# Kernel tuning notes

Measured on AMD Instinct MI355X. Metric: run time of the kernel, lower is better.

Reference implementation:

```python
import jax, jax.numpy as jnp
import numpy as np

B, D, O = 128, 1024, 512
EPS = 1e-5

def setup_inputs() -> dict:
    key = jax.random.key(0)
    ks = jax.random.split(key, 12)
    s = 0.02  # truncated-normal-ish scale
    glorot1 = float(np.sqrt(6.0 / (D + O)))
    glorot3 = float(np.sqrt(6.0 / (3 * O + O)))
    return {
        "x": jax.random.normal(ks[0], (B, D), jnp.float32),
        "gt": jax.random.normal(ks[1], (D, O), jnp.float32) * s,
        "wt": jax.random.normal(ks[2], (D, O), jnp.float32) * s,
        "mt": jax.random.normal(ks[3], (D, O), jnp.float32) * s,
        "kernel_1": jax.random.uniform(ks[4], (D, O), jnp.float32, -glorot1, glorot1),
        "bias_1": jnp.zeros((O,), jnp.float32),
        "kernel_3": jax.random.uniform(ks[5], (3 * O, O), jnp.float32, -glorot3, glorot3),
        "bias_3": jnp.zeros((O,), jnp.float32),
        "emb_kernel": jax.random.normal(ks[6], (1, 1, 3 * O), jnp.float32) * s,  # conv1d kernel [1, in=1, 3O]
        "emb_bias": jnp.zeros((3 * O,), jnp.float32),
        "embeding_k": jax.random.normal(ks[7], (1, D, 1), jnp.float32) * s,
        "norm_g": jnp.ones((O,), jnp.float32),
        "norm_b": jnp.zeros((O,), jnp.float32),
    }

def reference(x, gt, wt, mt, kernel_1, bias_1, kernel_3, bias_3,
              emb_kernel, emb_bias, embeding_k, norm_g, norm_b):
    # perceptron cell (identity activation)
    c1 = x @ kernel_1 + bias_1                                  # [B,O]
    # NALU cell
    wa = jnp.tanh(wt) * jax.nn.sigmoid(mt)                      # [D,O]
    g = jax.nn.sigmoid(x @ gt)                                  # [B,O]
    a = x @ wa                                                  # [B,O]
    m = jnp.sinh(jnp.arcsinh(x) @ wa)                           # [B,O]
    c3 = g * a + (1.0 - g) * m                                  # [B,O]
    # test cell: per-feature self-attention
    e = x[..., None] * emb_kernel.reshape(1, 1, -1) + emb_bias  # [B,D,3O]
    q, k, v = jnp.split(e, 3, axis=-1)                          # each [B,D,O]
    scale = jax.lax.rsqrt(jnp.asarray(v.shape[-1], x.dtype))
    w = jnp.einsum('bdo,beo->bde', q, k) * scale                # [B,D,D]
    w = jax.nn.softmax(w, axis=-1)
    att = jnp.einsum('bde,beo->bdo', w, v)                      # [B,D,O]
    s = jnp.sum(att * embeding_k, axis=1)                       # [B,O]
    u = jnp.mean(s, axis=-1, keepdims=True)
    var = jnp.mean(jnp.square(s - u), axis=-1, keepdims=True)
    c4 = (s - u) * jax.lax.rsqrt(var + EPS) * norm_g + norm_b   # [B,O]
    feat = jnp.concatenate([c1, c3, c4], axis=-1)               # [B,3O]
    return feat @ kernel_3 + bias_3                             # [B,O]
```

## Files before the change

### kernel.cpp

```cpp
#include <hip/hip_runtime.h>
#include <hip/hip_bf16.h>
#include <math.h>

typedef unsigned short u16;
typedef unsigned int u32;
typedef __attribute__((ext_vector_type(8))) short bf16x8;
typedef __attribute__((ext_vector_type(4))) float f32x4;

#define NB 128
#define ND 1024
#define NO 512
#define EPSV 1e-5f
#define SCALEQK 0.04419417382415922f
#define LOG2E 1.4426950408889634f

static __device__ __forceinline__ float fast_exp2(float v) {
#if __has_builtin(__builtin_amdgcn_exp2f)
  return __builtin_amdgcn_exp2f(v);
#else
  return exp2f(v);
#endif
}
static __device__ __forceinline__ float fast_rcp(float v) {
#if __has_builtin(__builtin_amdgcn_rcpf)
  return __builtin_amdgcn_rcpf(v);
#else
  return 1.f / v;
#endif
}
static __device__ __forceinline__ u16 bf16_rtn(float f) {
  unsigned u = __float_as_uint(f);
  return (u16)((u + 0x7FFFu + ((u >> 16) & 1u)) >> 16);
}
static __device__ __forceinline__ float asinh_fast(float x) {
  const float ax = fabsf(x);
  const float s = sqrtf(fmaf(ax, ax, 1.f));
  return copysignf(__logf(ax + s), x);
}
static __device__ __forceinline__ float tanh_fast(float x) {
  return 1.f - 2.f * fast_rcp(fast_exp2(x * (2.f * LOG2E)) + 1.f);
}
static __device__ __forceinline__ float sig_fast(float x) {
  return fast_rcp(1.f + fast_exp2(-x * LOG2E));
}
static __device__ __forceinline__ float sinh_fast(float x) {
  const float z = fast_exp2(x * LOG2E);
  return 0.5f * (z - fast_rcp(z));
}

template <int AMODE, int WMODE>
static __device__ __forceinline__ void gemmA_tile(
    const float* __restrict__ Xf, const float* __restrict__ W0,
    const float* __restrict__ W1, float* __restrict__ outp,
    int o0, int k0, char* smem) {
  u16* Ash = (u16*)smem;
  u16* Bsh = (u16*)(smem + 32768);
  const int t = threadIdx.x;
  const int lane = t & 63;
  const int wr = (t >> 6) & 3;
  const int wc = t >> 8;
  const f32x4 vz = {0.f, 0.f, 0.f, 0.f};
  f32x4 acc[2][2];
  acc[0][0] = vz; acc[0][1] = vz; acc[1][0] = vz; acc[1][1] = vz;

#pragma unroll
  for (int c = 0; c < 2; ++c) {
    const int kc = k0 + c * 128;
    if (c) __syncthreads();
    {
      const int rsub = t >> 5, c4 = (t & 31) * 4;
#pragma unroll
      for (int pass = 0; pass < 8; ++pass) {
        const int row = pass * 16 + rsub;
        const float4 v = *(const float4*)(Xf + (size_t)row * ND + kc + c4);
        float e[4] = {v.x, v.y, v.z, v.w};
        if (AMODE == 2) {
#pragma unroll
          for (int i = 0; i < 4; ++i) e[i] = asinh_fast(e[i]);
        }
        u16 h[4];
#pragma unroll
        for (int i = 0; i < 4; ++i) h[i] = bf16_rtn(e[i]);
        const int byte = (row * 256 + c4 * 2) ^ ((row & 7) << 4);
        *(uint2*)((char*)Ash + byte) =
            make_uint2((u32)h[0] | ((u32)h[1] << 16), (u32)h[2] | ((u32)h[3] << 16));
      }
    }
    {
      const int gkr = t >> 4, og = t & 15;
      const int go = o0 + og * 4;
#pragma unroll
      for (int kk = 0; kk < 4; ++kk) {
        const int gk = kc + gkr * 4 + kk;
        float4 w0 = *(const float4*)&W0[(size_t)gk * NO + go];
        if (WMODE) {
          const float4 m0 = *(const float4*)&W1[(size_t)gk * NO + go];
          w0.x = tanh_fast(w0.x) * sig_fast(m0.x);
          w0.y = tanh_fast(w0.y) * sig_fast(m0.y);
          w0.z = tanh_fast(w0.z) * sig_fast(m0.z);
          w0.w = tanh_fast(w0.w) * sig_fast(m0.w);
        }
        const float e[4] = {w0.x, w0.y, w0.z, w0.w};
#pragma unroll
        for (int j = 0; j < 4; ++j) {
          const int col = og * 4 + j;
          const int byte = (col * 256 + (gkr * 4 + kk) * 2) ^ ((col & 7) << 4);
          *(u16*)((char*)Bsh + byte) = bf16_rtn(e[j]);
        }
      }
    }
    __syncthreads();
#pragma unroll
    for (int ks2 = 0; ks2 < 4; ++ks2) {
      const int kbyte = ks2 * 64 + (lane >> 4) * 16;
      bf16x8 a[2], b[2];
#pragma unroll
      for (int m = 0; m < 2; ++m) {
        const int row = wr * 32 + m * 16 + (lane & 15);
        a[m] = *(const bf16x8*)((const char*)Ash + ((row * 256 + kbyte) ^ ((row & 7) << 4)));
      }
#pragma unroll
      for (int n = 0; n < 2; ++n) {
        const int col = wc * 32 + n * 16 + (lane & 15);
        b[n] = *(const bf16x8*)((const char*)Bsh + ((col * 256 + kbyte) ^ ((col & 7) << 4)));
      }
#pragma unroll
      for (int m = 0; m < 2; ++m)
#pragma unroll
        for (int n = 0; n < 2; ++n)
          acc[m][n] = __builtin_amdgcn_mfma_f32_16x16x32_bf16(a[m], b[n], acc[m][n], 0, 0, 0);
    }
  }
#pragma unroll
  for (int m = 0; m < 2; ++m)
#pragma unroll
    for (int n = 0; n < 2; ++n) {
      const int col = o0 + wc * 32 + n * 16 + (lane & 15);
#pragma unroll
      for (int r = 0; r < 4; ++r) {
        const int row = wr * 32 + m * 16 + (lane >> 4) * 4 + r;
        outp[(size_t)row * NO + col] = acc[m][n][r];
      }
    }
}

__global__ __launch_bounds__(512) void k1_fused(
    const float* __restrict__ x, const float* __restrict__ gt,
    const float* __restrict__ wt, const float* __restrict__ mt,
    const float* __restrict__ k1w, const float* __restrict__ embk,
    const float* __restrict__ embb, const float* __restrict__ ekd,
    const float* __restrict__ k3w, const float* __restrict__ ng,
    const float* __restrict__ nbv, float* __restrict__ Tfull,
    float* __restrict__ pA, float* __restrict__ U, float* __restrict__ V,
    float* __restrict__ Wc) {
  __shared__ __align__(16) char smem[49152];
  const int bid = blockIdx.x;
  const int t = threadIdx.x;
  const int wv = t >> 6;

  if (bid < NB) {
    float* xsh = (float*)smem;
    float(*red)[8] = (float(*)[8])(smem + 4096);
    float* bc = (float*)(smem + 4096 + 7 * 8 * 4);
    *(float2*)&xsh[t * 2] = *(const float2*)&x[bid * ND + t * 2];
    float s1, s3;
    {
      const float kk = embk[NO + t];
      s1 = embk[t] * kk;
      s3 = kk * embb[t];
    }
#pragma unroll
    for (int off = 32; off; off >>= 1) {
      s1 += __shfl_xor(s1, off);
      s3 += __shfl_xor(s3, off);
    }
    if ((t & 63) == 0) { red[0][wv] = s1; red[1][wv] = s3; }
    __syncthreads();
    if (t < 2) {
      float v = 0.f;
#pragma unroll
      for (int i = 0; i < 8; ++i) v += red[t][i];
      bc[t] = v;
    }
    __syncthreads();
    const float S1 = bc[0], S3 = bc[1];
    const float aL2 = SCALEQK * LOG2E * S3;
    const float dS1 = SCALEQK * S1;
    float mm[7];
#pragma unroll
    for (int k = 0; k < 7; ++k) mm[k] = 0.f;
#pragma unroll
    for (int j = 0; j < 2; ++j) {
      const float xe = xsh[t * 2 + j];
      float p = fast_exp2(aL2 * xe);
      mm[0] += p;
#pragma unroll
      for (int k = 1; k < 7; ++k) { p *= xe; mm[k] += p; }
    }
#pragma unroll
    for (int off = 32; off; off >>= 1)
#pragma unroll
      for (int k = 0; k < 7; ++k) mm[k] += __shfl_xor(mm[k], off);
    if ((t & 63) == 0)
#pragma unroll
      for (int k = 0; k < 7; ++k) red[k][wv] = mm[k];
    __syncthreads();
    if (t < 7) {
      float v = 0.f;
#pragma unroll
      for (int i = 0; i < 8; ++i) v += red[t][i];
      bc[2 + t] = v;
    }
    __syncthreads();
    const float invf[6] = {1.f, 1.f, 0.5f, 1.6666667e-1f, 4.1666668e-2f, 8.3333333e-3f};
    float cn[6], cd[6];
#pragma unroll
    for (int k = 0; k < 6; ++k) {
      cn[k] = bc[3 + k] * invf[k];
      cd[k] = bc[2 + k] * invf[k];
    }
    float Ta = 0.f;
#pragma unroll
    for (int j = 0; j < 2; ++j) {
      const int d = t * 2 + j;
      const float del = dS1 * xsh[d];
      float num = cn[5], den = cd[5];
#pragma unroll
      for (int k = 4; k >= 0; --k) {
        num = fmaf(num, del, cn[k]);
        den = fmaf(den, del, cd[k]);
      }
      Ta = fmaf(ekd[d], num / den, Ta);
    }
#pragma unroll
    for (int off = 32; off; off >>= 1) Ta += __shfl_xor(Ta, off);
    __syncthreads();
    if ((t & 63) == 0) red[0][wv] = Ta;
    __syncthreads();
    if (t == 0) {
      float v = 0.f;
#pragma unroll
      for (int i = 0; i < 8; ++i) v += red[0][i];
      Tfull[bid] = v;
    }
    return;
  }
  if (bid < 256) {
    const int b2 = bid - NB;
    const int g = b2 >> 5, ks = (b2 >> 3) & 3, ot = b2 & 7;
    float* outp = pA + (size_t)(g * 4 + ks) * (NB * NO);
    if (g == 0)
      gemmA_tile<1, 0>(x, k1w, k1w, outp, ot * 64, ks * 256, smem);
    else if (g == 1)
      gemmA_tile<1, 0>(x, gt, gt, outp, ot * 64, ks * 256, smem);
    else if (g == 2)
      gemmA_tile<1, 1>(x, wt, mt, outp, ot * 64, ks * 256, smem);
    else
      gemmA_tile<2, 1>(x, wt, mt, outp, ot * 64, ks * 256, smem);
    return;
  }
  {
    float(*lds)[64][3] = (float(*)[64][3])smem;
    __shared__ float mred[2][8];
    __shared__ float mbc[2];
    float svk = embk[2 * NO + t], svb = embb[2 * NO + t];
#pragma unroll
    for (int off = 32; off; off >>= 1) {
      svk += __shfl_xor(svk, off);
      svb += __shfl_xor(svb, off);
    }
    if ((t & 63) == 0) { mred[0][wv] = svk; mred[1][wv] = svb; }
    __syncthreads();
    if (t < 2) {
      float s = 0.f;
#pragma unroll
      for (int i = 0; i < 8; ++i) s += mred[t][i];
      mbc[t] = s * (1.f / (float)NO);
    }
    __syncthreads();
    const float mvk = mbc[0], mvb = mbc[1];
    const int jbase = (bid - 256) * 64;
    const int j = jbase + (t & 63);
    const int oc = t >> 6;
    float au = 0.f, av = 0.f, aw = 0.f;
#pragma unroll 4
    for (int oo = 0; oo < 64; ++oo) {
      const int o = oc * 64 + oo;
      const float kj = k3w[(size_t)(2 * NO + o) * NO + j];
      const float g = ng[o];
      au = fmaf((embk[2 * NO + o] - mvk) * g, kj, au);
      av = fmaf((embb[2 * NO + o] - mvb) * g, kj, av);
      aw = fmaf(nbv[o], kj, aw);
    }
    lds[oc][t & 63][0] = au;
    lds[oc][t & 63][1] = av;
    lds[oc][t & 63][2] = aw;
    __syncthreads();
    if (t < 64) {
      float su = 0.f, sv = 0.f, sw = 0.f;
#pragma unroll
      for (int cch = 0; cch < 8; ++cch) {
        su += lds[cch][t][0];
        sv += lds[cch][t][1];
        sw += lds[cch][t][2];
      }
      U[jbase + t] = su;
      V[jbase + t] = sv;
      Wc[jbase + t] = sw;
    }
  }
}

__global__ __launch_bounds__(512) void k2_combineA(
    const float* __restrict__ pA, const float* __restrict__ b1,
    const float* __restrict__ embk, const float* __restrict__ embb,
    const float* __restrict__ ekd, const float* __restrict__ Tfull,
    const float* __restrict__ U, const float* __restrict__ V,
    const float* __restrict__ Wc, const float* __restrict__ b3,
    u16* __restrict__ featB, float* __restrict__ out) {
  __shared__ float red6[6][8];
  __shared__ float bc6[6];
  const int b = blockIdx.x, t = threadIdx.x;
  const int wv = t >> 6;
  {
    const float vk = embk[2 * NO + t], vb = embb[2 * NO + t];
    float svk = vk, svb = vb, svk2 = vk * vk, svkvb = vk * vb, svb2 = vb * vb;
    float se = ekd[t] + ekd[t + 512];
#pragma unroll
    for (int off = 32; off; off >>= 1) {
      svk += __shfl_xor(svk, off); svb += __shfl_xor(svb, off);
      svk2 += __shfl_xor(svk2, off); svkvb += __shfl_xor(svkvb, off);
      svb2 += __shfl_xor(svb2, off); se += __shfl_xor(se, off);
    }
    if ((t & 63) == 0) {
      red6[0][wv] = svk; red6[1][wv] = svb; red6[2][wv] = svk2;
      red6[3][wv] = svkvb; red6[4][wv] = svb2; red6[5][wv] = se;
    }
    __syncthreads();
    if (t < 6) {
      float s = 0.f;
#pragma unroll
      for (int i = 0; i < 8; ++i) s += red6[t][i];
      bc6[t] = s;
    }
    __syncthreads();
  }
  const float inv_o = 1.f / (float)NO;
  const float mvk = bc6[0] * inv_o, mvb = bc6[1] * inv_o;
  const float Mvk2 = bc6[2] * inv_o - mvk * mvk;
  const float Mvkvb = bc6[3] * inv_o - mvk * mvb;
  const float Mvb2 = bc6[4] * inv_o - mvb * mvb;
  const float E = bc6[5];
  const float T = Tfull[b];
  const float var = T * T * Mvk2 + 2.f * T * E * Mvkvb + E * E * Mvb2;
  const float rs = rsqrtf(var + EPSV);
  const float aS = T * rs, cS = E * rs;

  const size_t off = (size_t)b * NO + t;
  float d1 = 0.f, d2 = 0.f, d3 = 0.f, d4 = 0.f;
#pragma unroll
  for (int s = 0; s < 4; ++s) {
    d1 += pA[(size_t)(0 * 4 + s) * (NB * NO) + off];
    d2 += pA[(size_t)(1 * 4 + s) * (NB * NO) + off];
    d3 += pA[(size_t)(2 * 4 + s) * (NB * NO) + off];
    d4 += pA[(size_t)(3 * 4 + s) * (NB * NO) + off];
  }
  const float c1v = d1 + b1[t];
  const float gg = sig_fast(d2);
  const float sh = sinh_fast(d4);
  const float c3v = fmaf(gg, d3 - sh, sh);
  featB[(size_t)b * ND + t] = bf16_rtn(c1v);
  featB[(size_t)b * ND + NO + t] = bf16_rtn(c3v);
  out[off] = fmaf(aS, U[t], fmaf(cS, V[t], b3[t] + Wc[t]));
}

__global__ __launch_bounds__(512) void k3_gemmB(
    const u16* __restrict__ featB, const float* __restrict__ k3w,
    float* __restrict__ out) {
  __shared__ __align__(16) char smem[32768];
  u16* Ash = (u16*)smem;
  u16* Bsh = (u16*)(smem + 16384);
  const int t = threadIdx.x;
  const int lane = t & 63;
  const int wr = (t >> 6) & 3;
  const int wc = t >> 8;
  const int rh = blockIdx.x >> 6, ks = (blockIdx.x >> 3) & 7, ot = blockIdx.x & 7;
  const int r0 = rh * 64, k0 = ks * 128, o0 = ot * 64;

#pragma unroll
  for (int p2 = 0; p2 < 2; ++p2) {
    const int s = t + p2 * 512;
    const int row = s >> 4, j8 = (s & 15) * 8;
    const uint4 v = *(const uint4*)(featB + (size_t)(r0 + row) * ND + k0 + j8);
    const int byte = (row * 256 + j8 * 2) ^ ((row & 7) << 4);
    *(uint4*)((char*)Ash + byte) = v;
  }
  {
    const int gkr = t >> 4, og = t & 15;
    const int go = o0 + og * 4;
#pragma unroll
    for (int kk = 0; kk < 4; ++kk) {
      const int gk = k0 + gkr * 4 + kk;
      const float4 w0 = *(const float4*)&k3w[(size_t)gk * NO + go];
      const float e[4] = {w0.x, w0.y, w0.z, w0.w};
#pragma unroll
      for (int j = 0; j < 4; ++j) {
        const int col = og * 4 + j;
        const int byte = (col * 256 + (gkr * 4 + kk) * 2) ^ ((col & 7) << 4);
        *(u16*)((char*)Bsh + byte) = bf16_rtn(e[j]);
      }
    }
  }
  __syncthreads();
  const f32x4 vz = {0.f, 0.f, 0.f, 0.f};
  f32x4 acc[2];
  acc[0] = vz; acc[1] = vz;
#pragma unroll
  for (int ks2 = 0; ks2 < 4; ++ks2) {
    const int kbyte = ks2 * 64 + (lane >> 4) * 16;
    const int row = wr * 16 + (lane & 15);
    const bf16x8 a = *(const bf16x8*)((const char*)Ash + ((row * 256 + kbyte) ^ ((row & 7) << 4)));
#pragma unroll
    for (int n = 0; n < 2; ++n) {
      const int col = wc * 32 + n * 16 + (lane & 15);
      const bf16x8 b = *(const bf16x8*)((const char*)Bsh + ((col * 256 + kbyte) ^ ((col & 7) << 4)));
      acc[n] = __builtin_amdgcn_mfma_f32_16x16x32_bf16(a, b, acc[n], 0, 0, 0);
    }
  }
#pragma unroll
  for (int n = 0; n < 2; ++n) {
    const int col = o0 + wc * 32 + n * 16 + (lane & 15);
#pragma unroll
    for (int r = 0; r < 4; ++r) {
      const int row = r0 + wr * 16 + (lane >> 4) * 4 + r;
      atomicAdd(&out[(size_t)row * NO + col], acc[n][r]);
    }
  }
}

extern "C" void kernel_launch(void* const* d_in, const int* in_sizes, int n_in,
                              void* d_out, int out_size, void* d_ws, size_t ws_size,
                              hipStream_t stream) {
  const float* x    = (const float*)d_in[0];
  const float* gt   = (const float*)d_in[1];
  const float* wt   = (const float*)d_in[2];
  const float* mt   = (const float*)d_in[3];
  const float* k1   = (const float*)d_in[4];
  const float* b1   = (const float*)d_in[5];
  const float* k3   = (const float*)d_in[6];
  const float* b3   = (const float*)d_in[7];
  const float* embk = (const float*)d_in[8];
  const float* embb = (const float*)d_in[9];
  const float* ekd  = (const float*)d_in[10];
  const float* ng   = (const float*)d_in[11];
  const float* nb   = (const float*)d_in[12];

  char* wsb = (char*)d_ws;
  float* Tfull = (float*)wsb;
  float* U  = (float*)(wsb + 4096);
  float* V  = (float*)(wsb + 8192);
  float* Wc = (float*)(wsb + 12288);
  float* pA = (float*)(wsb + (1u << 20));
  u16* featB = (u16*)(wsb + (6u << 20));
  float* out = (float*)d_out;

  hipLaunchKernelGGL(k1_fused, dim3(264), dim3(512), 0, stream,
                     x, gt, wt, mt, k1, embk, embb, ekd, k3, ng, nb,
                     Tfull, pA, U, V, Wc);
  hipLaunchKernelGGL(k2_combineA, dim3(128), dim3(512), 0, stream,
                     pA, b1, embk, embb, ekd, Tfull, U, V, Wc, b3, featB, out);
  hipLaunchKernelGGL(k3_gemmB, dim3(128), dim3(512), 0, stream,
                     featB, k3, out);
}
```

Baseline: 26.62 us.

## Fuse combine stage into final GEMM and widen LDS staging stores

Merges the split-K reduction, bias, NALU gating and layernorm-term computation into the final GEMM kernel. The A tile is now built directly from the partial sums, so the featB bf16 intermediate and one kernel launch go away. Output is zeroed with a memset, and the ks==0 blocks add the bias and attention terms through the atomics. The X and weight staging in the first GEMM also switch to wider 16-byte and 8-byte LDS stores. In exchange, each block now recomputes the partial-sum reduction for its slice, adds a memset launch, and only the ks==0 blocks do the extra normalisation work.

```diff
diff --git a/kernel.cpp b/kernel.cpp
--- a/kernel.cpp
+++ b/kernel.cpp
@@ -68,45 +68,54 @@
     const int kc = k0 + c * 128;
     if (c) __syncthreads();
     {
-      const int rsub = t >> 5, c4 = (t & 31) * 4;
-#pragma unroll
-      for (int pass = 0; pass < 8; ++pass) {
-        const int row = pass * 16 + rsub;
-        const float4 v = *(const float4*)(Xf + (size_t)row * ND + kc + c4);
-        float e[4] = {v.x, v.y, v.z, v.w};
+      const int rsub = t >> 4, c8 = (t & 15) * 8;
+#pragma unroll
+      for (int pass = 0; pass < 4; ++pass) {
+        const int row = pass * 32 + rsub;
+        const float4 v0 = *(const float4*)(Xf + (size_t)row * ND + kc + c8);
+        const float4 v1 = *(const float4*)(Xf + (size_t)row * ND + kc + c8 + 4);
+        float e[8] = {v0.x, v0.y, v0.z, v0.w, v1.x, v1.y, v1.z, v1.w};
         if (AMODE == 2) {
 #pragma unroll
-          for (int i = 0; i < 4; ++i) e[i] = asinh_fast(e[i]);
+          for (int i = 0; i < 8; ++i) e[i] = asinh_fast(e[i]);
         }
-        u16 h[4];
-#pragma unroll
-        for (int i = 0; i < 4; ++i) h[i] = bf16_rtn(e[i]);
-        const int byte = (row * 256 + c4 * 2) ^ ((row & 7) << 4);
-        *(uint2*)((char*)Ash + byte) =
-            make_uint2((u32)h[0] | ((u32)h[1] << 16), (u32)h[2] | ((u32)h[3] << 16));
+        u16 h[8];
+#pragma unroll
+        for (int i = 0; i < 8; ++i) h[i] = bf16_rtn(e[i]);
+        const int byte = (row * 256 + c8 * 2) ^ ((row & 7) << 4);
+        *(uint4*)((char*)Ash + byte) = make_uint4(
+            (u32)h[0] | ((u32)h[1] << 16), (u32)h[2] | ((u32)h[3] << 16),
+            (u32)h[4] | ((u32)h[5] << 16), (u32)h[6] | ((u32)h[7] << 16));
       }
     }
     {
       const int gkr = t >> 4, og = t & 15;
       const int go = o0 + og * 4;
+      float4 w[4];
 #pragma unroll
       for (int kk = 0; kk < 4; ++kk) {
         const int gk = kc + gkr * 4 + kk;
-        float4 w0 = *(const float4*)&W0[(size_t)gk * NO + go];
+        w[kk] = *(const float4*)&W0[(size_t)gk * NO + go];
         if (WMODE) {
-          const float4 m0 = *(const float4*)&W1[(size_t)gk * NO + go];
-          w0.x = tanh_fast(w0.x) * sig_fast(m0.x);
-          w0.y = tanh_fast(w0.y) * sig_fast(m0.y);
-          w0.z = tanh_fast(w0.z) * sig_fast(m0.z);
-          w0.w = tanh_fast(w0.w) * sig_fast(m0.w);
+          const float4 m = *(const float4*)&W1[(size_t)gk * NO + go];
+          w[kk].x = tanh_fast(w[kk].x) * sig_fast(m.x);
+          w[kk].y = tanh_fast(w[kk].y) * sig_fast(m.y);
+          w[kk].z = tanh_fast(w[kk].z) * sig_fast(m.z);
+          w[kk].w = tanh_fast(w[kk].w) * sig_fast(m.w);
         }
-        const float e[4] = {w0.x, w0.y, w0.z, w0.w};
-#pragma unroll
-        for (int j = 0; j < 4; ++j) {
-          const int col = og * 4 + j;
-          const int byte = (col * 256 + (gkr * 4 + kk) * 2) ^ ((col & 7) << 4);
-          *(u16*)((char*)Bsh + byte) = bf16_rtn(e[j]);
-        }
+      }
+      const float* wp0 = (const float*)&w[0];
+      const float* wp1 = (const float*)&w[1];
+      const float* wp2 = (const float*)&w[2];
+      const float* wp3 = (const float*)&w[3];
+#pragma unroll
+      for (int j = 0; j < 4; ++j) {
+        const u16 h0 = bf16_rtn(wp0[j]), h1 = bf16_rtn(wp1[j]);
+        const u16 h2 = bf16_rtn(wp2[j]), h3 = bf16_rtn(wp3[j]);
+        const int col = og * 4 + j;
+        const int byte = (col * 256 + gkr * 8) ^ ((col & 7) << 4);
+        *(uint2*)((char*)Bsh + byte) =
+            make_uint2((u32)h0 | ((u32)h1 << 16), (u32)h2 | ((u32)h3 << 16));
       }
     }
     __syncthreads();
@@ -311,18 +320,28 @@
   }
 }
 
-__global__ __launch_bounds__(512) void k2_combineA(
-    const float* __restrict__ pA, const float* __restrict__ b1,
-    const float* __restrict__ embk, const float* __restrict__ embb,
-    const float* __restrict__ ekd, const float* __restrict__ Tfull,
-    const float* __restrict__ U, const float* __restrict__ V,
-    const float* __restrict__ Wc, const float* __restrict__ b3,
-    u16* __restrict__ featB, float* __restrict__ out) {
+__global__ __launch_bounds__(512) void k2_gemmB_fused(
+    const float* __restrict__ pA, const float* __restrict__ b1v,
+    const float* __restrict__ k3w, const float* __restrict__ embk,
+    const float* __restrict__ embb, const float* __restrict__ ekd,
+    const float* __restrict__ Tfull, const float* __restrict__ U,
+    const float* __restrict__ V, const float* __restrict__ Wc,
+    const float* __restrict__ b3, float* __restrict__ out) {
+  __shared__ __align__(16) char smem[32768];
+  u16* Ash = (u16*)smem;
+  u16* Bsh = (u16*)(smem + 16384);
   __shared__ float red6[6][8];
   __shared__ float bc6[6];
-  const int b = blockIdx.x, t = threadIdx.x;
+  __shared__ float aSl[64];
+  __shared__ float cSl[64];
+  const int t = threadIdx.x;
   const int wv = t >> 6;
-  {
+  const int lane = t & 63;
+  const int wr = wv & 3, wc = wv >> 2;
+  const int rh = blockIdx.x >> 6, ks = (blockIdx.x >> 3) & 7, ot = blockIdx.x & 7;
+  const int r0 = rh * 64, k0 = ks * 128, o0 = ot * 64;
+
+  if (ks == 0) {
     const float vk = embk[2 * NO + t], vb = embb[2 * NO + t];
     float svk = vk, svb = vb, svk2 = vk * vk, svkvb = vk * vb, svb2 = vb * vb;
     float se = ekd[t] + ekd[t + 512];
@@ -344,71 +363,98 @@
       bc6[t] = s;
     }
     __syncthreads();
-  }
-  const float inv_o = 1.f / (float)NO;
-  const float mvk = bc6[0] * inv_o, mvb = bc6[1] * inv_o;
-  const float Mvk2 = bc6[2] * inv_o - mvk * mvk;
-  const float Mvkvb = bc6[3] * inv_o - mvk * mvb;
-  const float Mvb2 = bc6[4] * inv_o - mvb * mvb;
-  const float E = bc6[5];
-  const float T = Tfull[b];
-  const float var = T * T * Mvk2 + 2.f * T * E * Mvkvb + E * E * Mvb2;
-  const float rs = rsqrtf(var + EPSV);
-  const float aS = T * rs, cS = E * rs;
-
-  const size_t off = (size_t)b * NO + t;
-  float d1 = 0.f, d2 = 0.f, d3 = 0.f, d4 = 0.f;
-#pragma unroll
-  for (int s = 0; s < 4; ++s) {
-    d1 += pA[(size_t)(0 * 4 + s) * (NB * NO) + off];
-    d2 += pA[(size_t)(1 * 4 + s) * (NB * NO) + off];
-    d3 += pA[(size_t)(2 * 4 + s) * (NB * NO) + off];
-    d4 += pA[(size_t)(3 * 4 + s) * (NB * NO) + off];
-  }
-  const float c1v = d1 + b1[t];
-  const float gg = sig_fast(d2);
-  const float sh = sinh_fast(d4);
-  const float c3v = fmaf(gg, d3 - sh, sh);
-  featB[(size_t)b * ND + t] = bf16_rtn(c1v);
-  featB[(size_t)b * ND + NO + t] = bf16_rtn(c3v);
-  out[off] = fmaf(aS, U[t], fmaf(cS, V[t], b3[t] + Wc[t]));
-}
-
-__global__ __launch_bounds__(512) void k3_gemmB(
-    const u16* __restrict__ featB, const float* __restrict__ k3w,
-    float* __restrict__ out) {
-  __shared__ __align__(16) char smem[32768];
-  u16* Ash = (u16*)smem;
-  u16* Bsh = (u16*)(smem + 16384);
-  const int t = threadIdx.x;
-  const int lane = t & 63;
-  const int wr = (t >> 6) & 3;
-  const int wc = t >> 8;
-  const int rh = blockIdx.x >> 6, ks = (blockIdx.x >> 3) & 7, ot = blockIdx.x & 7;
-  const int r0 = rh * 64, k0 = ks * 128, o0 = ot * 64;
-
-#pragma unroll
-  for (int p2 = 0; p2 < 2; ++p2) {
-    const int s = t + p2 * 512;
-    const int row = s >> 4, j8 = (s & 15) * 8;
-    const uint4 v = *(const uint4*)(featB + (size_t)(r0 + row) * ND + k0 + j8);
-    const int byte = (row * 256 + j8 * 2) ^ ((row & 7) << 4);
-    *(uint4*)((char*)Ash + byte) = v;
+    const float inv_o = 1.f / (float)NO;
+    const float mvk = bc6[0] * inv_o, mvb = bc6[1] * inv_o;
+    const float Mvk2 = bc6[2] * inv_o - mvk * mvk;
+    const float Mvkvb = bc6[3] * inv_o - mvk * mvb;
+    const float Mvb2 = bc6[4] * inv_o - mvb * mvb;
+    const float E = bc6[5];
+    if (t < 64) {
+      const float T = Tfull[r0 + t];
+      const float var = T * T * Mvk2 + 2.f * T * E * Mvkvb + E * E * Mvb2;
+      const float rs = rsqrtf(var + EPSV);
+      aSl[t] = T * rs;
+      cSl[t] = E * rs;
+    }
+    __syncthreads();
+  }
+
+  {
+    const int row = t >> 3;
+    const int jj = (t & 7) * 16;
+    const int j = k0 + jj;
+    const size_t rowoff = (size_t)(r0 + row) * NO;
+    float e[16];
+    if (ks < 4) {
+#pragma unroll
+      for (int q = 0; q < 4; ++q) {
+        float4 d = *(const float4*)&pA[rowoff + j + q * 4];
+#pragma unroll
+        for (int s = 1; s < 4; ++s) {
+          const float4 v = *(const float4*)&pA[(size_t)s * (NB * NO) + rowoff + j + q * 4];
+          d.x += v.x; d.y += v.y; d.z += v.z; d.w += v.w;
+        }
+        const float4 bb = *(const float4*)&b1v[j + q * 4];
+        e[q * 4 + 0] = d.x + bb.x; e[q * 4 + 1] = d.y + bb.y;
+        e[q * 4 + 2] = d.z + bb.z; e[q * 4 + 3] = d.w + bb.w;
+      }
+    } else {
+      const int o = j - NO;
+#pragma unroll
+      for (int q = 0; q < 4; ++q) {
+        float4 d2 = {0, 0, 0, 0}, d3 = {0, 0, 0, 0}, d4 = {0, 0, 0, 0};
+#pragma unroll
+        for (int s = 0; s < 4; ++s) {
+          const size_t base = rowoff + o + q * 4;
+          const float4 v2 = *(const float4*)&pA[(size_t)(4 + s) * (NB * NO) + base];
+          const float4 v3 = *(const float4*)&pA[(size_t)(8 + s) * (NB * NO) + base];
+          const float4 v4 = *(const float4*)&pA[(size_t)(12 + s) * (NB * NO) + base];
+          d2.x += v2.x; d2.y += v2.y; d2.z += v2.z; d2.w += v2.w;
+          d3.x += v3.x; d3.y += v3.y; d3.z += v3.z; d3.w += v3.w;
+          d4.x += v4.x; d4.y += v4.y; d4.z += v4.z; d4.w += v4.w;
+        }
+        const float g0 = sig_fast(d2.x), g1 = sig_fast(d2.y);
+        const float g2 = sig_fast(d2.z), g3 = sig_fast(d2.w);
+        const float s0 = sinh_fast(d4.x), s1 = sinh_fast(d4.y);
+        const float s2 = sinh_fast(d4.z), s3 = sinh_fast(d4.w);
+        e[q * 4 + 0] = fmaf(g0, d3.x - s0, s0);
+        e[q * 4 + 1] = fmaf(g1, d3.y - s1, s1);
+        e[q * 4 + 2] = fmaf(g2, d3.z - s2, s2);
+        e[q * 4 + 3] = fmaf(g3, d3.w - s3, s3);
+      }
+    }
+    u16 h[16];
+#pragma unroll
+    for (int i = 0; i < 16; ++i) h[i] = bf16_rtn(e[i]);
+    const int swz = (row & 7) << 4;
+    const int byte0 = (row * 256 + jj * 2) ^ swz;
+    const int byte1 = (row * 256 + jj * 2 + 16) ^ swz;
+    *(uint4*)((char*)Ash + byte0) = make_uint4(
+        (u32)h[0] | ((u32)h[1] << 16), (u32)h[2] | ((u32)h[3] << 16),
+        (u32)h[4] | ((u32)h[5] << 16), (u32)h[6] | ((u32)h[7] << 16));
+    *(uint4*)((char*)Ash + byte1) = make_uint4(
+        (u32)h[8] | ((u32)h[9] << 16), (u32)h[10] | ((u32)h[11] << 16),
+        (u32)h[12] | ((u32)h[13] << 16), (u32)h[14] | ((u32)h[15] << 16));
   }
   {
     const int gkr = t >> 4, og = t & 15;
     const int go = o0 + og * 4;
-#pragma unroll
-    for (int kk = 0; kk < 4; ++kk) {
-      const int gk = k0 + gkr * 4 + kk;
-      const float4 w0 = *(const float4*)&k3w[(size_t)gk * NO + go];
-      const float e[4] = {w0.x, w0.y, w0.z, w0.w};
-#pragma unroll
-      for (int j = 0; j < 4; ++j) {
-        const int col = og * 4 + j;
-        const int byte = (col * 256 + (gkr * 4 + kk) * 2) ^ ((col & 7) << 4);
-        *(u16*)((char*)Bsh + byte) = bf16_rtn(e[j]);
-      }
+    float4 w[4];
+#pragma unroll
+    for (int kk = 0; kk < 4; ++kk)
+      w[kk] = *(const float4*)&k3w[(size_t)(k0 + gkr * 4 + kk) * NO + go];
+    const float* wp0 = (const float*)&w[0];
+    const float* wp1 = (const float*)&w[1];
+    const float* wp2 = (const float*)&w[2];
+    const float* wp3 = (const float*)&w[3];
+#pragma unroll
+    for (int j = 0; j < 4; ++j) {
+      const u16 h0 = bf16_rtn(wp0[j]), h1 = bf16_rtn(wp1[j]);
+      const u16 h2 = bf16_rtn(wp2[j]), h3 = bf16_rtn(wp3[j]);
+      const int col = og * 4 + j;
+      const int byte = (col * 256 + gkr * 8) ^ ((col & 7) << 4);
+      *(uint2*)((char*)Bsh + byte) =
+          make_uint2((u32)h0 | ((u32)h1 << 16), (u32)h2 | ((u32)h3 << 16));
     }
   }
   __syncthreads();
@@ -430,10 +476,14 @@
 #pragma unroll
   for (int n = 0; n < 2; ++n) {
     const int col = o0 + wc * 32 + n * 16 + (lane & 15);
+    float base = 0.f, uc = 0.f, vc = 0.f;
+    if (ks == 0) { base = b3[col] + Wc[col]; uc = U[col]; vc = V[col]; }
 #pragma unroll
     for (int r = 0; r < 4; ++r) {
-      const int row = r0 + wr * 16 + (lane >> 4) * 4 + r;
-      atomicAdd(&out[(size_t)row * NO + col], acc[n][r]);
+      const int rl = wr * 16 + (lane >> 4) * 4 + r;
+      float add = acc[n][r];
+      if (ks == 0) add += fmaf(aSl[rl], uc, fmaf(cSl[rl], vc, base));
+      atomicAdd(&out[(size_t)(r0 + rl) * NO + col], add);
     }
   }
 }
@@ -461,14 +511,12 @@
   float* V  = (float*)(wsb + 8192);
   float* Wc = (float*)(wsb + 12288);
   float* pA = (float*)(wsb + (1u << 20));
-  u16* featB = (u16*)(wsb + (6u << 20));
   float* out = (float*)d_out;
 
+  hipMemsetAsync(out, 0, (size_t)out_size * sizeof(float), stream);
   hipLaunchKernelGGL(k1_fused, dim3(264), dim3(512), 0, stream,
                      x, gt, wt, mt, k1, embk, embb, ekd, k3, ng, nb,
                      Tfull, pA, U, V, Wc);
-  hipLaunchKernelGGL(k2_combineA, dim3(128), dim3(512), 0, stream,
-                     pA, b1, embk, embb, ekd, Tfull, U, V, Wc, b3, featB, out);
-  hipLaunchKernelGGL(k3_gemmB, dim3(128), dim3(512), 0, stream,
-                     featB, k3, out);
-}
+  hipLaunchKernelGGL(k2_gemmB_fused, dim3(128), dim3(512), 0, stream,
+                     pA, b1, k3, embk, embb, ekd, Tfull, U, V, Wc, b3, out);
+}
```

Result: slower. 38.61 us (+45.0%).

## Split GEMM-A K across 8 slices, batch global loads, and vectorize LDS stores

Applied to the files above, without the earlier changes.

The first-stage GEMM tiles now cover K=128 instead of K=256, which doubles the GEMM block count from 128 to 256 and the grid from 264 to 392. Each tile issues all its global loads up front, then converts and writes to LDS with wider packed stores (uint4 for A, uint2 for transposed B instead of per-element u16). The combine kernel loads 8 partial sums per output, batched before reduction, and the workspace offset for featB moves to fit the larger partial buffer. k3 gets the same load-batching and packed B stores. The aim is more parallelism and memory-level overlap, at the cost of twice the partial-sum traffic and redundant transcendental work on X per slice.

```diff
diff --git a/kernel.cpp b/kernel.cpp
--- a/kernel.cpp
+++ b/kernel.cpp
@@ -59,77 +59,88 @@
   const int lane = t & 63;
   const int wr = (t >> 6) & 3;
   const int wc = t >> 8;
+
+  const int rsub = t >> 4, c8 = (t & 15) * 8;
+  float4 va[4], vb[4];
+#pragma unroll
+  for (int pass = 0; pass < 4; ++pass) {
+    const size_t rowoff = (size_t)(pass * 32 + rsub) * ND + k0 + c8;
+    va[pass] = *(const float4*)(Xf + rowoff);
+    vb[pass] = *(const float4*)(Xf + rowoff + 4);
+  }
+  const int gkr = t >> 4, og = t & 15;
+  const int go = o0 + og * 4;
+  float4 w[4], mw[4];
+#pragma unroll
+  for (int kk = 0; kk < 4; ++kk) {
+    w[kk] = *(const float4*)&W0[(size_t)(k0 + gkr * 4 + kk) * NO + go];
+    if (WMODE) mw[kk] = *(const float4*)&W1[(size_t)(k0 + gkr * 4 + kk) * NO + go];
+  }
+
+#pragma unroll
+  for (int pass = 0; pass < 4; ++pass) {
+    const int row = pass * 32 + rsub;
+    float e[8] = {va[pass].x, va[pass].y, va[pass].z, va[pass].w,
+                  vb[pass].x, vb[pass].y, vb[pass].z, vb[pass].w};
+    if (AMODE == 2) {
+#pragma unroll
+      for (int i = 0; i < 8; ++i) e[i] = asinh_fast(e[i]);
+    }
+    u16 h[8];
+#pragma unroll
+    for (int i = 0; i < 8; ++i) h[i] = bf16_rtn(e[i]);
+    const int byte = (row * 256 + c8 * 2) ^ ((row & 7) << 4);
+    *(uint4*)((char*)Ash + byte) = make_uint4(
+        (u32)h[0] | ((u32)h[1] << 16), (u32)h[2] | ((u32)h[3] << 16),
+        (u32)h[4] | ((u32)h[5] << 16), (u32)h[6] | ((u32)h[7] << 16));
+  }
+  {
+    if (WMODE) {
+#pragma unroll
+      for (int kk = 0; kk < 4; ++kk) {
+        w[kk].x = tanh_fast(w[kk].x) * sig_fast(mw[kk].x);
+        w[kk].y = tanh_fast(w[kk].y) * sig_fast(mw[kk].y);
+        w[kk].z = tanh_fast(w[kk].z) * sig_fast(mw[kk].z);
+        w[kk].w = tanh_fast(w[kk].w) * sig_fast(mw[kk].w);
+      }
+    }
+    const float* wp0 = (const float*)&w[0];
+    const float* wp1 = (const float*)&w[1];
+    const float* wp2 = (const float*)&w[2];
+    const float* wp3 = (const float*)&w[3];
+#pragma unroll
+    for (int j = 0; j < 4; ++j) {
+      const u16 h0 = bf16_rtn(wp0[j]), h1 = bf16_rtn(wp1[j]);
+      const u16 h2 = bf16_rtn(wp2[j]), h3 = bf16_rtn(wp3[j]);
+      const int col = og * 4 + j;
+      const int byte = (col * 256 + gkr * 8) ^ ((col & 7) << 4);
+      *(uint2*)((char*)Bsh + byte) =
+          make_uint2((u32)h0 | ((u32)h1 << 16), (u32)h2 | ((u32)h3 << 16));
+    }
+  }
+  __syncthreads();
   const f32x4 vz = {0.f, 0.f, 0.f, 0.f};
   f32x4 acc[2][2];
   acc[0][0] = vz; acc[0][1] = vz; acc[1][0] = vz; acc[1][1] = vz;
-
-#pragma unroll
-  for (int c = 0; c < 2; ++c) {
-    const int kc = k0 + c * 128;
-    if (c) __syncthreads();
-    {
-      const int rsub = t >> 5, c4 = (t & 31) * 4;
-#pragma unroll
-      for (int pass = 0; pass < 8; ++pass) {
-        const int row = pass * 16 + rsub;
-        const float4 v = *(const float4*)(Xf + (size_t)row * ND + kc + c4);
-        float e[4] = {v.x, v.y, v.z, v.w};
-        if (AMODE == 2) {
-#pragma unroll
-          for (int i = 0; i < 4; ++i) e[i] = asinh_fast(e[i]);
-        }
-        u16 h[4];
-#pragma unroll
-        for (int i = 0; i < 4; ++i) h[i] = bf16_rtn(e[i]);
-        const int byte = (row * 256 + c4 * 2) ^ ((row & 7) << 4);
-        *(uint2*)((char*)Ash + byte) =
-            make_uint2((u32)h[0] | ((u32)h[1] << 16), (u32)h[2] | ((u32)h[3] << 16));
-      }
-    }
-    {
-      const int gkr = t >> 4, og = t & 15;
-      const int go = o0 + og * 4;
-#pragma unroll
-      for (int kk = 0; kk < 4; ++kk) {
-        const int gk = kc + gkr * 4 + kk;
-        float4 w0 = *(const float4*)&W0[(size_t)gk * NO + go];
-        if (WMODE) {
-          const float4 m0 = *(const float4*)&W1[(size_t)gk * NO + go];
-          w0.x = tanh_fast(w0.x) * sig_fast(m0.x);
-          w0.y = tanh_fast(w0.y) * sig_fast(m0.y);
-          w0.z = tanh_fast(w0.z) * sig_fast(m0.z);
-          w0.w = tanh_fast(w0.w) * sig_fast(m0.w);
-        }
-        const float e[4] = {w0.x, w0.y, w0.z, w0.w};
-#pragma unroll
-        for (int j = 0; j < 4; ++j) {
-          const int col = og * 4 + j;
-          const int byte = (col * 256 + (gkr * 4 + kk) * 2) ^ ((col & 7) << 4);
-          *(u16*)((char*)Bsh + byte) = bf16_rtn(e[j]);
-        }
-      }
-    }
-    __syncthreads();
-#pragma unroll
-    for (int ks2 = 0; ks2 < 4; ++ks2) {
-      const int kbyte = ks2 * 64 + (lane >> 4) * 16;
-      bf16x8 a[2], b[2];
-#pragma unroll
-      for (int m = 0; m < 2; ++m) {
-        const int row = wr * 32 + m * 16 + (lane & 15);
-        a[m] = *(const bf16x8*)((const char*)Ash + ((row * 256 + kbyte) ^ ((row & 7) << 4)));
-      }
-#pragma unroll
-      for (int n = 0; n < 2; ++n) {
-        const int col = wc * 32 + n * 16 + (lane & 15);
-        b[n] = *(const bf16x8*)((const char*)Bsh + ((col * 256 + kbyte) ^ ((col & 7) << 4)));
-      }
-#pragma unroll
-      for (int m = 0; m < 2; ++m)
-#pragma unroll
-        for (int n = 0; n < 2; ++n)
-          acc[m][n] = __builtin_amdgcn_mfma_f32_16x16x32_bf16(a[m], b[n], acc[m][n], 0, 0, 0);
-    }
+#pragma unroll
+  for (int ks2 = 0; ks2 < 4; ++ks2) {
+    const int kbyte = ks2 * 64 + (lane >> 4) * 16;
+    bf16x8 a[2], b[2];
+#pragma unroll
+    for (int m = 0; m < 2; ++m) {
+      const int row = wr * 32 + m * 16 + (lane & 15);
+      a[m] = *(const bf16x8*)((const char*)Ash + ((row * 256 + kbyte) ^ ((row & 7) << 4)));
+    }
+#pragma unroll
+    for (int n = 0; n < 2; ++n) {
+      const int col = wc * 32 + n * 16 + (lane & 15);
+      b[n] = *(const bf16x8*)((const char*)Bsh + ((col * 256 + kbyte) ^ ((col & 7) << 4)));
+    }
+#pragma unroll
+    for (int m = 0; m < 2; ++m)
+#pragma unroll
+      for (int n = 0; n < 2; ++n)
+        acc[m][n] = __builtin_amdgcn_mfma_f32_16x16x32_bf16(a[m], b[n], acc[m][n], 0, 0, 0);
   }
 #pragma unroll
   for (int m = 0; m < 2; ++m)
@@ -245,18 +256,18 @@
     }
     return;
   }
-  if (bid < 256) {
+  if (bid < 384) {
     const int b2 = bid - NB;
-    const int g = b2 >> 5, ks = (b2 >> 3) & 3, ot = b2 & 7;
-    float* outp = pA + (size_t)(g * 4 + ks) * (NB * NO);
+    const int g = b2 >> 6, ks = (b2 >> 3) & 7, ot = b2 & 7;
+    float* outp = pA + (size_t)(g * 8 + ks) * (NB * NO);
     if (g == 0)
-      gemmA_tile<1, 0>(x, k1w, k1w, outp, ot * 64, ks * 256, smem);
+      gemmA_tile<1, 0>(x, k1w, k1w, outp, ot * 64, ks * 128, smem);
     else if (g == 1)
-      gemmA_tile<1, 0>(x, gt, gt, outp, ot * 64, ks * 256, smem);
+      gemmA_tile<1, 0>(x, gt, gt, outp, ot * 64, ks * 128, smem);
     else if (g == 2)
-      gemmA_tile<1, 1>(x, wt, mt, outp, ot * 64, ks * 256, smem);
+      gemmA_tile<1, 1>(x, wt, mt, outp, ot * 64, ks * 128, smem);
     else
-      gemmA_tile<2, 1>(x, wt, mt, outp, ot * 64, ks * 256, smem);
+      gemmA_tile<2, 1>(x, wt, mt, outp, ot * 64, ks * 128, smem);
     return;
   }
   {
@@ -279,7 +290,7 @@
     }
     __syncthreads();
     const float mvk = mbc[0], mvb = mbc[1];
-    const int jbase = (bid - 256) * 64;
+    const int jbase = (bid - 384) * 64;
     const int j = jbase + (t & 63);
     const int oc = t >> 6;
     float au = 0.f, av = 0.f, aw = 0.f;
@@ -357,14 +368,17 @@
   const float aS = T * rs, cS = E * rs;
 
   const size_t off = (size_t)b * NO + t;
+  float v1[8], v2[8], v3[8], v4[8];
+#pragma unroll
+  for (int s = 0; s < 8; ++s) {
+    v1[s] = pA[(size_t)(0 * 8 + s) * (NB * NO) + off];
+    v2[s] = pA[(size_t)(1 * 8 + s) * (NB * NO) + off];
+    v3[s] = pA[(size_t)(2 * 8 + s) * (NB * NO) + off];
+    v4[s] = pA[(size_t)(3 * 8 + s) * (NB * NO) + off];
+  }
   float d1 = 0.f, d2 = 0.f, d3 = 0.f, d4 = 0.f;
 #pragma unroll
-  for (int s = 0; s < 4; ++s) {
-    d1 += pA[(size_t)(0 * 4 + s) * (NB * NO) + off];
-    d2 += pA[(size_t)(1 * 4 + s) * (NB * NO) + off];
-    d3 += pA[(size_t)(2 * 4 + s) * (NB * NO) + off];
-    d4 += pA[(size_t)(3 * 4 + s) * (NB * NO) + off];
-  }
+  for (int s = 0; s < 8; ++s) { d1 += v1[s]; d2 += v2[s]; d3 += v3[s]; d4 += v4[s]; }
   const float c1v = d1 + b1[t];
   const float gg = sig_fast(d2);
   const float sh = sinh_fast(d4);
@@ -387,28 +401,40 @@
   const int rh = blockIdx.x >> 6, ks = (blockIdx.x >> 3) & 7, ot = blockIdx.x & 7;
   const int r0 = rh * 64, k0 = ks * 128, o0 = ot * 64;
 
+  uint4 av[2];
 #pragma unroll
   for (int p2 = 0; p2 < 2; ++p2) {
     const int s = t + p2 * 512;
     const int row = s >> 4, j8 = (s & 15) * 8;
-    const uint4 v = *(const uint4*)(featB + (size_t)(r0 + row) * ND + k0 + j8);
+    av[p2] = *(const uint4*)(featB + (size_t)(r0 + row) * ND + k0 + j8);
+  }
+  const int gkr = t >> 4, og = t & 15;
+  const int go = o0 + og * 4;
+  float4 w[4];
+#pragma unroll
+  for (int kk = 0; kk < 4; ++kk)
+    w[kk] = *(const float4*)&k3w[(size_t)(k0 + gkr * 4 + kk) * NO + go];
+
+#pragma unroll
+  for (int p2 = 0; p2 < 2; ++p2) {
+    const int s = t + p2 * 512;
+    const int row = s >> 4, j8 = (s & 15) * 8;
     const int byte = (row * 256 + j8 * 2) ^ ((row & 7) << 4);
-    *(uint4*)((char*)Ash + byte) = v;
+    *(uint4*)((char*)Ash + byte) = av[p2];
   }
   {
-    const int gkr = t >> 4, og = t & 15;
-    const int go = o0 + og * 4;
-#pragma unroll
-    for (int kk = 0; kk < 4; ++kk) {
-      const int gk = k0 + gkr * 4 + kk;
-      const float4 w0 = *(const float4*)&k3w[(size_t)gk * NO + go];
-      const float e[4] = {w0.x, w0.y, w0.z, w0.w};
-#pragma unroll
-      for (int j = 0; j < 4; ++j) {
-        const int col = og * 4 + j;
-        const int byte = (col * 256 + (gkr * 4 + kk) * 2) ^ ((col & 7) << 4);
-        *(u16*)((char*)Bsh + byte) = bf16_rtn(e[j]);
-      }
+    const float* wp0 = (const float*)&w[0];
+    const float* wp1 = (const float*)&w[1];
+    const float* wp2 = (const float*)&w[2];
+    const float* wp3 = (const float*)&w[3];
+#pragma unroll
+    for (int j = 0; j < 4; ++j) {
+      const u16 h0 = bf16_rtn(wp0[j]), h1 = bf16_rtn(wp1[j]);
+      const u16 h2 = bf16_rtn(wp2[j]), h3 = bf16_rtn(wp3[j]);
+      const int col = og * 4 + j;
+      const int byte = (col * 256 + gkr * 8) ^ ((col & 7) << 4);
+      *(uint2*)((char*)Bsh + byte) =
+          make_uint2((u32)h0 | ((u32)h1 << 16), (u32)h2 | ((u32)h3 << 16));
     }
   }
   __syncthreads();
@@ -461,10 +487,10 @@
   float* V  = (float*)(wsb + 8192);
   float* Wc = (float*)(wsb + 12288);
   float* pA = (float*)(wsb + (1u << 20));
-  u16* featB = (u16*)(wsb + (6u << 20));
+  u16* featB = (u16*)(wsb + (10u << 20));
   float* out = (float*)d_out;
 
-  hipLaunchKernelGGL(k1_fused, dim3(264), dim3(512), 0, stream,
+  hipLaunchKernelGGL(k1_fused, dim3(392), dim3(512), 0, stream,
                      x, gt, wt, mt, k1, embk, embb, ekd, k3, ng, nb,
                      Tfull, pA, U, V, Wc);
   hipLaunchKernelGGL(k2_combineA, dim3(128), dim3(512), 0, stream,
```

Result: faster. 24.61 us (-7.6%).
